# Optimization experiments

Hardware: AMD Instinct MI355X
Metric: run time of the kernel (lower is better)

The kernel has to match this reference:

```python
import jax, jax.numpy as jnp
import numpy as np

N_NODES = 100000
N_EDGES = 1600000
IN_DIM = 128
HID = 128
N_CLASSES = 10
N_GRAPHS = 64


def setup_inputs() -> dict:
    key = jax.random.key(0)
    ks = jax.random.split(key, 12)
    x = jax.random.normal(ks[0], (N_NODES, IN_DIM), dtype=jnp.float32)
    edge_index = jax.random.randint(ks[1], (2, N_EDGES), 0, N_NODES, dtype=jnp.int64)
    batch = jnp.sort(jax.random.randint(ks[2], (N_NODES,), 0, N_GRAPHS, dtype=jnp.int64))
    s = 1.0 / np.sqrt(HID)
    W_gcn = jax.random.uniform(ks[3], (IN_DIM, HID), jnp.float32, -s, s)
    b_gcn = jnp.zeros((HID,), jnp.float32)
    w_ih = jax.random.uniform(ks[4], (4 * HID, HID), jnp.float32, -s, s)
    w_hh = jax.random.uniform(ks[5], (4 * HID, HID), jnp.float32, -s, s)
    b_ih = jax.random.uniform(ks[6], (4 * HID,), jnp.float32, -s, s)
    b_hh = jax.random.uniform(ks[7], (4 * HID,), jnp.float32, -s, s)
    W_fc = jax.random.uniform(ks[8], (N_CLASSES, HID), jnp.float32, -s, s)
    b_fc = jax.random.uniform(ks[9], (N_CLASSES,), jnp.float32, -s, s)
    return dict(x=x, edge_index=edge_index, batch=batch, W_gcn=W_gcn, b_gcn=b_gcn,
                w_ih=w_ih, w_hh=w_hh, b_ih=b_ih, b_hh=b_hh, W_fc=W_fc, b_fc=b_fc)


def _gcn_conv(x, edge_index, W, b):
    # PyG GCNConv: add self-loops, symmetric norm D^-1/2 (A+I) D^-1/2, then bias.
    row, col = edge_index[0], edge_index[1]
    ones = jnp.ones((edge_index.shape[1],), x.dtype)
    deg = jax.ops.segment_sum(ones, col, num_segments=N_NODES) + 1.0  # +1 for self-loop
    dinv = jax.lax.rsqrt(deg)
    xt = x @ W  # [N, HID]
    norm = dinv[row] * dinv[col]  # [E]
    agg = jax.ops.segment_sum(xt[row] * norm[:, None], col, num_segments=N_NODES)
    agg = agg + xt * (dinv * dinv)[:, None]  # self-loop contribution
    return agg + b


def _lstm(seq, w_ih, w_hh, b_ih, b_hh):
    # torch LSTM gate order: i, f, g, o
    def step(carry, x_t):
        h, c = carry
        gates = x_t @ w_ih.T + h @ w_hh.T + b_ih + b_hh
        i, f, g, o = jnp.split(gates, 4)
        c = jax.nn.sigmoid(f) * c + jax.nn.sigmoid(i) * jnp.tanh(g)
        h = jax.nn.sigmoid(o) * jnp.tanh(c)
        return (h, c), h
    h0 = jnp.zeros((HID,), seq.dtype)
    (_, _), hs = jax.lax.scan(step, (h0, h0), seq)
    return hs  # [T, HID]


def reference(x, edge_index, batch, W_gcn, b_gcn, w_ih, w_hh, b_ih, b_hh, W_fc, b_fc):
    h = jax.nn.relu(_gcn_conv(x, edge_index, W_gcn, b_gcn))
    # dropout is identity at inference
    sums = jax.ops.segment_sum(h, batch, num_segments=N_GRAPHS)
    cnt = jax.ops.segment_sum(jnp.ones((N_NODES,), h.dtype), batch, num_segments=N_GRAPHS)
    pooled = sums / jnp.maximum(cnt, 1.0)[:, None]  # [G, HID]
    hs = _lstm(pooled, w_ih, w_hh, b_ih, b_hh)  # [G, HID]
    return hs @ W_fc.T + b_fc  # [G, N_CLASSES]
```

## Files before the change

kernel.cpp:

```cpp
#include <hip/hip_runtime.h>
#include <hip/hip_fp16.h>
#include <math.h>

#if __has_builtin(__builtin_amdgcn_cvt_pk_f32_fp8) && __has_builtin(__builtin_amdgcn_cvt_pk_fp8_f32)
#define HAS_FP8_CVT 1
#else
#include <hip/hip_fp8.h>
#endif

#define NNODES 100000
#define NEDGES 1600000
#define DIM 128
#define NG 64
#define GATE 512
#define SCAN_NB 98
#define FILL_NPASS 4
#define BUCKET ((NNODES + FILL_NPASS - 1) / FILL_NPASS)

#define HG 128
#define HW 25024
#define HSMEM (HW * 4)

#define SMEM_W   131072
#define SMEM_AUX (256 + 2048 + 16384)
#define SMEM_TOTAL (SMEM_W + SMEM_AUX)

typedef _Float16 f16x2 __attribute__((ext_vector_type(2)));
typedef _Float16 half8_t __attribute__((ext_vector_type(8)));
typedef float f32x4 __attribute__((ext_vector_type(4)));
typedef float f32x2_t __attribute__((ext_vector_type(2)));

__device__ __forceinline__ f16x2 f2h2cast(float f) {
    union U { float f; f16x2 h; } u; u.f = f; return u.h;
}
__device__ __forceinline__ float fdot2f(f16x2 a, f16x2 b, float c) {
#if __has_builtin(__builtin_amdgcn_fdot2)
    return __builtin_amdgcn_fdot2(a, b, c, false);
#else
    return c + (float)a[0] * (float)b[0] + (float)a[1] * (float)b[1];
#endif
}

__device__ __forceinline__ unsigned char f32_to_fp8(float v) {
#ifdef HAS_FP8_CVT
    return (unsigned char)(__builtin_amdgcn_cvt_pk_fp8_f32(v, v, 0, false) & 0xFF);
#else
    __hip_fp8_e4m3 h(v); return h.__x;
#endif
}
__device__ __forceinline__ void fp8x4_acc(unsigned w, float* acc) {
#ifdef HAS_FP8_CVT
    f32x2_t lo = __builtin_amdgcn_cvt_pk_f32_fp8((int)w, false);
    f32x2_t hi = __builtin_amdgcn_cvt_pk_f32_fp8((int)w, true);
    acc[0] += lo[0]; acc[1] += lo[1]; acc[2] += hi[0]; acc[3] += hi[1];
#else
    __hip_fp8_e4m3 h;
#pragma unroll
    for (int q = 0; q < 4; ++q) { h.__x = (w >> (8 * q)) & 0xFF; acc[q] += (float)h; }
#endif
}

__device__ __forceinline__ float sigf(float x) {
    return __builtin_amdgcn_rcpf(1.0f + __expf(-x));
}
__device__ __forceinline__ float tanhfast(float x) {
    float e = __expf(2.0f * x);
    return 1.0f - 2.0f * __builtin_amdgcn_rcpf(e + 1.0f);
}

__global__ __launch_bounds__(1024) void k_deghist(const int* __restrict__ ei, unsigned* __restrict__ partial) {
    extern __shared__ unsigned hist[];
    int tid = threadIdx.x;
    for (int i = tid; i < HW; i += 1024) hist[i] = 0u;
    __syncthreads();
    int e0 = blockIdx.x * (NEDGES / HG);
    int e1 = e0 + (NEDGES / HG);
    for (int e = e0 + tid; e < e1; e += 1024) {
        int col = ei[NEDGES + e];
        atomicAdd(&hist[col >> 2], 1u << ((col & 3) * 8));
    }
    __syncthreads();
    unsigned* dst = partial + (size_t)blockIdx.x * HW;
    for (int i = tid; i < HW; i += 1024) dst[i] = hist[i];
}

__global__ __launch_bounds__(256) void k_deg(const int* __restrict__ ei, int* __restrict__ deg) {
    int e = blockIdx.x * 256 + threadIdx.x;
    if (e < NEDGES) atomicAdd(&deg[ei[NEDGES + e]], 1);
}

__global__ __launch_bounds__(256) void k_degred(const unsigned* __restrict__ partial, int* __restrict__ deg,
                                                float* __restrict__ dinv) {
    int w = blockIdx.x * 256 + threadIdx.x;
    if (w >= NNODES / 4) return;
    unsigned s = 0;
    for (int b = 0; b < HG; ++b) s += partial[(size_t)b * HW + w];
    int4 d;
    d.x = s & 255; d.y = (s >> 8) & 255; d.z = (s >> 16) & 255; d.w = (int)(s >> 24);
    ((int4*)deg)[w] = d;
    float4 dv;
    dv.x = rsqrtf((float)d.x + 1.f);
    dv.y = rsqrtf((float)d.y + 1.f);
    dv.z = rsqrtf((float)d.z + 1.f);
    dv.w = rsqrtf((float)d.w + 1.f);
    ((float4*)dinv)[w] = dv;
}

__global__ __launch_bounds__(256) void k_dinv(const int* __restrict__ deg, float* __restrict__ dinv) {
    int n = blockIdx.x * 256 + threadIdx.x;
    if (n < NNODES) dinv[n] = rsqrtf((float)deg[n] + 1.0f);
}

__global__ __launch_bounds__(1024) void k_scan1(const int* __restrict__ deg, int* __restrict__ row_ptr,
                                                int* __restrict__ bsum) {
    __shared__ int ls[1024];
    int tid = threadIdx.x;
    int n = blockIdx.x * 1024 + tid;
    int v = (n < NNODES) ? deg[n] : 0;
    ls[tid] = v;
    __syncthreads();
    for (int off = 1; off < 1024; off <<= 1) {
        int t = (tid >= off) ? ls[tid - off] : 0;
        __syncthreads();
        ls[tid] += t;
        __syncthreads();
    }
    if (n < NNODES) row_ptr[n] = ls[tid] - v;
    if (tid == 1023) bsum[blockIdx.x] = ls[1023];
}

__global__ __launch_bounds__(128) void k_scan2(int* __restrict__ bsum, int* __restrict__ row_ptr,
                                               const int* __restrict__ batch, int* __restrict__ start) {
    __shared__ int ls[128];
    int tid = threadIdx.x;
    int v = (tid < SCAN_NB) ? bsum[tid] : 0;
    ls[tid] = v;
    __syncthreads();
    for (int off = 1; off < 128; off <<= 1) {
        int t = (tid >= off) ? ls[tid - off] : 0;
        __syncthreads();
        ls[tid] += t;
        __syncthreads();
    }
    if (tid < SCAN_NB) bsum[tid] = ls[tid] - v;
    if (tid == 127) row_ptr[NNODES] = ls[127];
    if (tid <= NG) {
        int lo = 0, hi = NNODES;
        while (lo < hi) {
            int mid = (lo + hi) >> 1;
            if (batch[mid] < tid) lo = mid + 1; else hi = mid;
        }
        start[tid] = lo;
    }
}

__global__ __launch_bounds__(1024) void k_scan3(int* __restrict__ row_ptr, const int* __restrict__ bsum,
                                                int* __restrict__ cursor) {
    int n = blockIdx.x * 1024 + threadIdx.x;
    if (n < NNODES) {
        int rp = row_ptr[n] + bsum[blockIdx.x];
        row_ptr[n] = rp;
        cursor[n] = rp;
    }
}

__global__ __launch_bounds__(256) void k_fillb(const int* __restrict__ ei, int* __restrict__ cursor,
                                               int* __restrict__ adj, int b0) {
    int e = blockIdx.x * 256 + threadIdx.x;
    if (e < NEDGES) {
        int col = ei[NEDGES + e];
        if (col >= b0 && col < b0 + BUCKET) {
            int row = ei[e];
            int pos = atomicAdd(&cursor[col], 1);
            adj[pos] = row;
        }
    }
}

__global__ __launch_bounds__(256) void k_wprep(const float* __restrict__ W_gcn, const float* __restrict__ w_hh,
                                               __half* __restrict__ Wt, __half* __restrict__ whh16) {
    int t = blockIdx.x * 256 + threadIdx.x;
    if (t < GATE * DIM) {
        whh16[t] = __float2half(w_hh[t]);
    } else {
        int idx = t - GATE * DIM;
        if (idx < DIM * DIM) {
            int d = idx >> 7, k = idx & 127;
            Wt[idx] = __float2half(W_gcn[k * DIM + d]);
        }
    }
}

__global__ __launch_bounds__(256) void k_gemmm(const float* __restrict__ x, const __half* __restrict__ Wt,
                                               const float* __restrict__ dinv, unsigned char* __restrict__ yf8) {
    int tid = threadIdx.x;
    int wt = tid >> 6, lane = tid & 63;
    int lr = lane & 15, kgrp = lane >> 4;
    int rb = blockIdx.x * 64 + wt * 16;

    int rowA = rb + lr;
    if (rowA >= NNODES) rowA = NNODES - 1;
    const float4* x4 = (const float4*)x;

    f32x4 acc[8];
#pragma unroll
    for (int ct = 0; ct < 8; ++ct) acc[ct] = (f32x4){0.f, 0.f, 0.f, 0.f};

#pragma unroll
    for (int c = 0; c < 4; ++c) {
        int kb = c * 32 + kgrp * 8;
        float4 v0 = x4[(size_t)rowA * 32 + (kb >> 2)];
        float4 v1 = x4[(size_t)rowA * 32 + (kb >> 2) + 1];
        half8_t a;
        a[0] = (_Float16)v0.x; a[1] = (_Float16)v0.y; a[2] = (_Float16)v0.z; a[3] = (_Float16)v0.w;
        a[4] = (_Float16)v1.x; a[5] = (_Float16)v1.y; a[6] = (_Float16)v1.z; a[7] = (_Float16)v1.w;
#pragma unroll
        for (int ct = 0; ct < 8; ++ct) {
            int col = ct * 16 + lr;
            half8_t b = *(const half8_t*)(Wt + (size_t)col * DIM + kb);
            acc[ct] = __builtin_amdgcn_mfma_f32_16x16x32_f16(a, b, acc[ct], 0, 0, 0);
        }
    }

    int rowbase = rb + kgrp * 4;
    float dv[4];
    bool ok[4];
#pragma unroll
    for (int r = 0; r < 4; ++r) {
        int row = rowbase + r;
        ok[r] = row < NNODES;
        dv[r] = ok[r] ? dinv[row] : 0.f;
    }
#pragma unroll
    for (int ct = 0; ct < 8; ++ct) {
#pragma unroll
        for (int r = 0; r < 4; ++r) {
            if (ok[r])
                yf8[(size_t)(rowbase + r) * DIM + ct * 16 + lr] = f32_to_fp8(acc[ct][r] * dv[r]);
        }
    }
}

__global__ __launch_bounds__(256) void k_gpool(const int* __restrict__ row_ptr, const int* __restrict__ adj,
                                               const uint2* __restrict__ Y, const float* __restrict__ dinv,
                                               const float* __restrict__ bias, const int* __restrict__ batch,
                                               float* __restrict__ sums) {
    __shared__ float red[16][132];
    __shared__ int gid[16];
    int tid = threadIdx.x;
    int sl = tid >> 4;
    int l = tid & 15;
    int n = blockIdx.x * 16 + sl;

    int s = row_ptr[n], e = row_ptr[n + 1];
    float acc[8];
#pragma unroll
    for (int q = 0; q < 8; ++q) acc[q] = 0.f;
    {
        uint2 v = Y[(size_t)n * 16 + l];
        fp8x4_acc(v.x, acc);
        fp8x4_acc(v.y, acc + 4);
    }
    int i = s;
    for (; i + 3 < e; i += 4) {
        int r0 = adj[i], r1 = adj[i + 1], r2 = adj[i + 2], r3 = adj[i + 3];
        uint2 a0 = Y[(size_t)r0 * 16 + l];
        uint2 a1 = Y[(size_t)r1 * 16 + l];
        uint2 a2 = Y[(size_t)r2 * 16 + l];
        uint2 a3 = Y[(size_t)r3 * 16 + l];
        fp8x4_acc(a0.x, acc); fp8x4_acc(a0.y, acc + 4);
        fp8x4_acc(a1.x, acc); fp8x4_acc(a1.y, acc + 4);
        fp8x4_acc(a2.x, acc); fp8x4_acc(a2.y, acc + 4);
        fp8x4_acc(a3.x, acc); fp8x4_acc(a3.y, acc + 4);
    }
    for (; i < e; ++i) {
        uint2 a0 = Y[(size_t)adj[i] * 16 + l];
        fp8x4_acc(a0.x, acc); fp8x4_acc(a0.y, acc + 4);
    }

    float dv = dinv[n];
#pragma unroll
    for (int q = 0; q < 8; ++q) {
        float v = dv * acc[q] + bias[l * 8 + q];
        red[sl][l * 8 + q] = fmaxf(v, 0.f);
    }
    if (l == 0) gid[sl] = batch[n];
    __syncthreads();

    if (tid < DIM) {
        int d = tid;
        float a = 0.f;
        int g = gid[0];
        for (int s2 = 0; s2 < 16; ++s2) {
            int gs = gid[s2];
            if (gs != g) {
                if (a != 0.f) atomicAdd(&sums[g * DIM + d], a);
                a = 0.f; g = gs;
            }
            a += red[s2][d];
        }
        if (a != 0.f) atomicAdd(&sums[g * DIM + d], a);
    }
}

__global__ __launch_bounds__(512) void k_xgate(const float* __restrict__ sums, const int* __restrict__ start,
                                               const float* __restrict__ w_ih, const float* __restrict__ b_ih,
                                               const float* __restrict__ b_hh, float* __restrict__ xg) {
    __shared__ float4 p4[DIM / 4];
    int t = blockIdx.x, j = threadIdx.x;
    if (j < DIM) {
        int c = start[t + 1] - start[t];
        float inv = 1.0f / fmaxf((float)c, 1.0f);
        ((float*)p4)[j] = sums[t * DIM + j] * inv;
    }
    __syncthreads();
    const float4* w4 = (const float4*)(w_ih + (size_t)j * DIM);
    float acc = b_ih[j] + b_hh[j];
#pragma unroll
    for (int kk = 0; kk < 32; ++kk) {
        float4 w = w4[kk];
        float4 p = p4[kk];
        acc += w.x * p.x + w.y * p.y + w.z * p.z + w.w * p.w;
    }
    xg[t * GATE + j] = acc;
}

template <int LDSW>
__global__ __launch_bounds__(512) void k_lstm2(const float* __restrict__ xg, const __half* __restrict__ whh16,
                                               const float* __restrict__ Wfc, const float* __restrict__ bfc,
                                               float* __restrict__ out) {
    extern __shared__ char smem[];
    half8_t* w8L = (half8_t*)smem;
    char* aux = LDSW ? (smem + SMEM_W) : smem;
    __half* h2h = (__half*)aux;
    float* gates = (float*)(aux + 256);
    __half* hsh = (__half*)(aux + 256 + 2048);
    int j = threadIdx.x;
    int sw = j & 15;

    if (LDSW) {
#pragma unroll
        for (int c = 0; c < 16; ++c) {
            half8_t g = *(const half8_t*)(whh16 + (size_t)j * DIM + 8 * c);
            w8L[j * 16 + (c ^ sw)] = g;
        }
    }
    if (j < DIM) h2h[j] = __float2half(0.f);
    float c = 0.f;
    float xcur = xg[j];
    __syncthreads();

    const half8_t* wrow = LDSW ? (const half8_t*)w8L : (const half8_t*)whh16;
    const float4* h4 = (const float4*)h2h;
    for (int t = 0; t < NG; ++t) {
        float xnext = (t + 1 < NG) ? xg[(t + 1) * GATE + j] : 0.f;
        float acc = xcur;
#pragma unroll
        for (int cc = 0; cc < 16; ++cc) {
            int idx = LDSW ? (j * 16 + (cc ^ sw)) : (j * 16 + cc);
            union { half8_t v; f16x2 p[4]; } w;
            w.v = wrow[idx];
            float4 hr = h4[cc];
            acc = fdot2f(w.p[0], f2h2cast(hr.x), acc);
            acc = fdot2f(w.p[1], f2h2cast(hr.y), acc);
            acc = fdot2f(w.p[2], f2h2cast(hr.z), acc);
            acc = fdot2f(w.p[3], f2h2cast(hr.w), acc);
        }
        gates[j] = acc;
        __syncthreads();
        if (j < DIM) {
            float gi = gates[j], gf = gates[DIM + j], gg = gates[2 * DIM + j], go = gates[3 * DIM + j];
            c = sigf(gf) * c + sigf(gi) * tanhfast(gg);
            float hn = sigf(go) * tanhfast(c);
            h2h[j] = __float2half(hn);
            hsh[t * DIM + j] = __float2half(hn);
        }
        xcur = xnext;
        __syncthreads();
    }

    for (int o = j; o < NG * 10; o += 512) {
        int t = o / 10, cls = o - t * 10;
        const __half2* hv = (const __half2*)(hsh + t * DIM);
        float acc = bfc[cls];
#pragma unroll
        for (int kk = 0; kk < 64; ++kk) {
            float2 hf = __half22float2(hv[kk]);
            acc += hf.x * Wfc[cls * DIM + 2 * kk] + hf.y * Wfc[cls * DIM + 2 * kk + 1];
        }
        out[o] = acc;
    }
}

extern "C" void kernel_launch(void* const* d_in, const int* in_sizes, int n_in,
                              void* d_out, int out_size, void* d_ws, size_t ws_size,
                              hipStream_t stream) {
    const float* x     = (const float*)d_in[0];
    const int*   ei    = (const int*)d_in[1];
    const int*   batch = (const int*)d_in[2];
    const float* W_gcn = (const float*)d_in[3];
    const float* b_gcn = (const float*)d_in[4];
    const float* w_ih  = (const float*)d_in[5];
    const float* w_hh  = (const float*)d_in[6];
    const float* b_ih  = (const float*)d_in[7];
    const float* b_hh  = (const float*)d_in[8];
    const float* W_fc  = (const float*)d_in[9];
    const float* b_fc  = (const float*)d_in[10];
    float* out = (float*)d_out;

    char* ws = (char*)d_ws;
    unsigned char* yf8 = (unsigned char*)ws;
    __half* wt16  = (__half*)(ws + (size_t)NNODES * DIM * 2);
    unsigned* partial = (unsigned*)(ws + (size_t)NNODES * DIM * 2 + (1 << 16));
    float*  dinv  = (float*)(ws + (size_t)NNODES * DIM * 4);
    float*  sums  = dinv + 100096;
    float*  xg    = sums + NG * DIM;
    int*    deg   = (int*)(xg + NG * GATE);
    int*    row_ptr = deg + 100096;
    int*    cursor  = row_ptr + 100096;
    int*    adj     = cursor + 100096;
    int*    start   = adj + NEDGES;
    int*    bsum    = start + 128;
    __half* whh16   = (__half*)(bsum + 128);

    hipMemsetAsync(sums, 0, NG * DIM * sizeof(float), stream);

    bool hist_ok = hipFuncSetAttribute((const void*)k_deghist,
                                       hipFuncAttributeMaxDynamicSharedMemorySize,
                                       HSMEM) == hipSuccess;
    if (hist_ok) {
        k_deghist<<<HG, 1024, HSMEM, stream>>>(ei, partial);
        k_degred<<<(NNODES / 4 + 255) / 256, 256, 0, stream>>>(partial, deg, dinv);
    } else {
        hipMemsetAsync(deg, 0, NNODES * sizeof(int), stream);
        k_deg<<<(NEDGES + 255) / 256, 256, 0, stream>>>(ei, deg);
        k_dinv<<<(NNODES + 255) / 256, 256, 0, stream>>>(deg, dinv);
    }
    k_scan1<<<SCAN_NB, 1024, 0, stream>>>(deg, row_ptr, bsum);
    k_scan2<<<1, 128, 0, stream>>>(bsum, row_ptr, batch, start);
    k_scan3<<<SCAN_NB, 1024, 0, stream>>>(row_ptr, bsum, cursor);
    for (int p = 0; p < FILL_NPASS; ++p)
        k_fillb<<<(NEDGES + 255) / 256, 256, 0, stream>>>(ei, cursor, adj, p * BUCKET);
    k_wprep<<<(GATE * DIM + DIM * DIM + 255) / 256, 256, 0, stream>>>(W_gcn, w_hh, wt16, whh16);
    k_gemmm<<<(NNODES + 63) / 64, 256, 0, stream>>>(x, wt16, dinv, yf8);
    k_gpool<<<NNODES / 16, 256, 0, stream>>>(row_ptr, adj, (const uint2*)yf8, dinv, b_gcn, batch, sums);
    k_xgate<<<NG, 512, 0, stream>>>(sums, start, w_ih, b_ih, b_hh, xg);

    bool lds_ok = hipFuncSetAttribute((const void*)k_lstm2<1>,
                                      hipFuncAttributeMaxDynamicSharedMemorySize,
                                      SMEM_TOTAL) == hipSuccess;
    if (lds_ok)
        k_lstm2<1><<<1, 512, SMEM_TOTAL, stream>>>(xg, whh16, W_fc, b_fc, out);
    else
        k_lstm2<0><<<1, 512, SMEM_AUX, stream>>>(xg, whh16, W_fc, b_fc, out);
}
```

Before: 283.6 us.

## Replace atomic CSR fill with per-block prefix fill; use MFMA for LSTM recurrence

The degree-reduction kernel now also stores, for each histogram block, an exclusive prefix of the per-block 8-bit degree counts. A new fill kernel uses that prefix plus LDS atomics to place edges into adj, replacing the global cursor atomics. Separately, the single-block LSTM recurrence switches from fdot2 over LDS-staged weights to 16x16x32 f16 MFMA, with w_hh held in registers and h broadcast as row 0 of the A matrix. This removes global atomic contention and the serial dot-product latency, at the cost of wasted MFMA rows and extra workspace traffic for pre8.

Result: faster. 236.2 us (-16.7%).

```diff
diff --git a/kernel.cpp b/kernel.cpp
--- a/kernel.cpp
+++ b/kernel.cpp
@@ -21,25 +21,9 @@
 #define HW 25024
 #define HSMEM (HW * 4)
 
-#define SMEM_W   131072
-#define SMEM_AUX (256 + 2048 + 16384)
-#define SMEM_TOTAL (SMEM_W + SMEM_AUX)
-
-typedef _Float16 f16x2 __attribute__((ext_vector_type(2)));
 typedef _Float16 half8_t __attribute__((ext_vector_type(8)));
 typedef float f32x4 __attribute__((ext_vector_type(4)));
 typedef float f32x2_t __attribute__((ext_vector_type(2)));
-
-__device__ __forceinline__ f16x2 f2h2cast(float f) {
-    union U { float f; f16x2 h; } u; u.f = f; return u.h;
-}
-__device__ __forceinline__ float fdot2f(f16x2 a, f16x2 b, float c) {
-#if __has_builtin(__builtin_amdgcn_fdot2)
-    return __builtin_amdgcn_fdot2(a, b, c, false);
-#else
-    return c + (float)a[0] * (float)b[0] + (float)a[1] * (float)b[1];
-#endif
-}
 
 __device__ __forceinline__ unsigned char f32_to_fp8(float v) {
 #ifdef HAS_FP8_CVT
@@ -89,12 +73,15 @@
     if (e < NEDGES) atomicAdd(&deg[ei[NEDGES + e]], 1);
 }
 
-__global__ __launch_bounds__(256) void k_degred(const unsigned* __restrict__ partial, int* __restrict__ deg,
-                                                float* __restrict__ dinv) {
+__global__ __launch_bounds__(256) void k_degred2(const unsigned* __restrict__ partial, unsigned* __restrict__ pre8,
+                                                 int* __restrict__ deg, float* __restrict__ dinv) {
     int w = blockIdx.x * 256 + threadIdx.x;
     if (w >= NNODES / 4) return;
     unsigned s = 0;
-    for (int b = 0; b < HG; ++b) s += partial[(size_t)b * HW + w];
+    for (int b = 0; b < HG; ++b) {
+        pre8[(size_t)b * HW + w] = s;
+        s += partial[(size_t)b * HW + w];
+    }
     int4 d;
     d.x = s & 255; d.y = (s >> 8) & 255; d.z = (s >> 16) & 255; d.w = (int)(s >> 24);
     ((int4*)deg)[w] = d;
@@ -161,6 +148,28 @@
         int rp = row_ptr[n] + bsum[blockIdx.x];
         row_ptr[n] = rp;
         cursor[n] = rp;
+    }
+}
+
+__global__ __launch_bounds__(1024) void k_fill2(const int* __restrict__ ei, const int* __restrict__ row_ptr,
+                                                const unsigned* __restrict__ pre8, int* __restrict__ adj, int b0) {
+    __shared__ unsigned lh[BUCKET / 4];
+    int tid = threadIdx.x;
+    for (int i = tid; i < BUCKET / 4; i += 1024) lh[i] = 0u;
+    __syncthreads();
+    const unsigned* myPre = pre8 + (size_t)blockIdx.x * HW;
+    int e0 = blockIdx.x * (NEDGES / HG);
+    int e1 = e0 + (NEDGES / HG);
+    for (int e = e0 + tid; e < e1; e += 1024) {
+        int col = ei[NEDGES + e];
+        if (col >= b0 && col < b0 + BUCKET) {
+            int row = ei[e];
+            int lc = col - b0;
+            unsigned old = atomicAdd(&lh[lc >> 2], 1u << ((lc & 3) * 8));
+            int local = (old >> ((lc & 3) * 8)) & 0xFF;
+            int base = row_ptr[col] + (int)((myPre[col >> 2] >> ((col & 3) * 8)) & 0xFF);
+            adj[base + local] = row;
+        }
     }
 }
 
@@ -325,61 +334,70 @@
     xg[t * GATE + j] = acc;
 }
 
-template <int LDSW>
-__global__ __launch_bounds__(512) void k_lstm2(const float* __restrict__ xg, const __half* __restrict__ whh16,
+__global__ __launch_bounds__(512) void k_lstmm(const float* __restrict__ xg, const __half* __restrict__ whh16,
                                                const float* __restrict__ Wfc, const float* __restrict__ bfc,
                                                float* __restrict__ out) {
-    extern __shared__ char smem[];
-    half8_t* w8L = (half8_t*)smem;
-    char* aux = LDSW ? (smem + SMEM_W) : smem;
-    __half* h2h = (__half*)aux;
-    float* gates = (float*)(aux + 256);
-    __half* hsh = (__half*)(aux + 256 + 2048);
-    int j = threadIdx.x;
-    int sw = j & 15;
-
-    if (LDSW) {
-#pragma unroll
-        for (int c = 0; c < 16; ++c) {
-            half8_t g = *(const half8_t*)(whh16 + (size_t)j * DIM + 8 * c);
-            w8L[j * 16 + (c ^ sw)] = g;
-        }
-    }
-    if (j < DIM) h2h[j] = __float2half(0.f);
+    __shared__ __half h2h[DIM];
+    __shared__ float gates[GATE];
+    __shared__ __half hsh[NG * DIM];
+    int tid = threadIdx.x;
+    int wid = tid >> 6, lane = tid & 63;
+    int lr = lane & 15, kg = lane >> 4;
+    int colbase = wid * 64;
+
+    half8_t bf[4][4];
+#pragma unroll
+    for (int ct = 0; ct < 4; ++ct)
+#pragma unroll
+        for (int ks = 0; ks < 4; ++ks)
+            bf[ct][ks] = *(const half8_t*)(whh16 + (size_t)(colbase + ct * 16 + lr) * DIM + ks * 32 + kg * 8);
+
+    if (tid < DIM) h2h[tid] = __float2half(0.f);
     float c = 0.f;
-    float xcur = xg[j];
-    __syncthreads();
-
-    const half8_t* wrow = LDSW ? (const half8_t*)w8L : (const half8_t*)whh16;
-    const float4* h4 = (const float4*)h2h;
+    float xc[4], xn[4];
+#pragma unroll
+    for (int ct = 0; ct < 4; ++ct) xc[ct] = xg[colbase + ct * 16 + lr];
+    __syncthreads();
+
     for (int t = 0; t < NG; ++t) {
-        float xnext = (t + 1 < NG) ? xg[(t + 1) * GATE + j] : 0.f;
-        float acc = xcur;
-#pragma unroll
-        for (int cc = 0; cc < 16; ++cc) {
-            int idx = LDSW ? (j * 16 + (cc ^ sw)) : (j * 16 + cc);
-            union { half8_t v; f16x2 p[4]; } w;
-            w.v = wrow[idx];
-            float4 hr = h4[cc];
-            acc = fdot2f(w.p[0], f2h2cast(hr.x), acc);
-            acc = fdot2f(w.p[1], f2h2cast(hr.y), acc);
-            acc = fdot2f(w.p[2], f2h2cast(hr.z), acc);
-            acc = fdot2f(w.p[3], f2h2cast(hr.w), acc);
-        }
-        gates[j] = acc;
-        __syncthreads();
-        if (j < DIM) {
-            float gi = gates[j], gf = gates[DIM + j], gg = gates[2 * DIM + j], go = gates[3 * DIM + j];
+        half8_t a[4];
+#pragma unroll
+        for (int ks = 0; ks < 4; ++ks) {
+            half8_t av = {};
+            if (lr == 0) av = *(const half8_t*)(h2h + ks * 32 + kg * 8);
+            a[ks] = av;
+        }
+        f32x4 acc[4];
+#pragma unroll
+        for (int ct = 0; ct < 4; ++ct) {
+            f32x4 z = (f32x4){0.f, 0.f, 0.f, 0.f};
+            if (lane < 16) z[0] = xc[ct];
+            acc[ct] = z;
+#pragma unroll
+            for (int ks = 0; ks < 4; ++ks)
+                acc[ct] = __builtin_amdgcn_mfma_f32_16x16x32_f16(a[ks], bf[ct][ks], acc[ct], 0, 0, 0);
+        }
+        int tn = (t + 1 < NG) ? t + 1 : t;
+#pragma unroll
+        for (int ct = 0; ct < 4; ++ct) xn[ct] = xg[tn * GATE + colbase + ct * 16 + lr];
+        if (lane < 16) {
+#pragma unroll
+            for (int ct = 0; ct < 4; ++ct) gates[colbase + ct * 16 + lane] = acc[ct][0];
+        }
+        __syncthreads();
+        if (tid < DIM) {
+            float gi = gates[tid], gf = gates[DIM + tid], gg = gates[2 * DIM + tid], go = gates[3 * DIM + tid];
             c = sigf(gf) * c + sigf(gi) * tanhfast(gg);
             float hn = sigf(go) * tanhfast(c);
-            h2h[j] = __float2half(hn);
-            hsh[t * DIM + j] = __float2half(hn);
-        }
-        xcur = xnext;
-        __syncthreads();
-    }
-
-    for (int o = j; o < NG * 10; o += 512) {
+            h2h[tid] = __float2half(hn);
+            hsh[t * DIM + tid] = __float2half(hn);
+        }
+#pragma unroll
+        for (int ct = 0; ct < 4; ++ct) xc[ct] = xn[ct];
+        __syncthreads();
+    }
+
+    for (int o = tid; o < NG * 10; o += 512) {
         int t = o / 10, cls = o - t * 10;
         const __half2* hv = (const __half2*)(hsh + t * DIM);
         float acc = bfc[cls];
@@ -410,6 +428,7 @@
 
     char* ws = (char*)d_ws;
     unsigned char* yf8 = (unsigned char*)ws;
+    unsigned* pre8 = (unsigned*)(ws + (size_t)NNODES * DIM);
     __half* wt16  = (__half*)(ws + (size_t)NNODES * DIM * 2);
     unsigned* partial = (unsigned*)(ws + (size_t)NNODES * DIM * 2 + (1 << 16));
     float*  dinv  = (float*)(ws + (size_t)NNODES * DIM * 4);
@@ -430,7 +449,7 @@
                                        HSMEM) == hipSuccess;
     if (hist_ok) {
         k_deghist<<<HG, 1024, HSMEM, stream>>>(ei, partial);
-        k_degred<<<(NNODES / 4 + 255) / 256, 256, 0, stream>>>(partial, deg, dinv);
+        k_degred2<<<(NNODES / 4 + 255) / 256, 256, 0, stream>>>(partial, pre8, deg, dinv);
     } else {
         hipMemsetAsync(deg, 0, NNODES * sizeof(int), stream);
         k_deg<<<(NEDGES + 255) / 256, 256, 0, stream>>>(ei, deg);
@@ -439,18 +458,16 @@
     k_scan1<<<SCAN_NB, 1024, 0, stream>>>(deg, row_ptr, bsum);
     k_scan2<<<1, 128, 0, stream>>>(bsum, row_ptr, batch, start);
     k_scan3<<<SCAN_NB, 1024, 0, stream>>>(row_ptr, bsum, cursor);
-    for (int p = 0; p < FILL_NPASS; ++p)
-        k_fillb<<<(NEDGES + 255) / 256, 256, 0, stream>>>(ei, cursor, adj, p * BUCKET);
+    if (hist_ok) {
+        for (int p = 0; p < FILL_NPASS; ++p)
+            k_fill2<<<HG, 1024, 0, stream>>>(ei, row_ptr, pre8, adj, p * BUCKET);
+    } else {
+        for (int p = 0; p < FILL_NPASS; ++p)
+            k_fillb<<<(NEDGES + 255) / 256, 256, 0, stream>>>(ei, cursor, adj, p * BUCKET);
+    }
     k_wprep<<<(GATE * DIM + DIM * DIM + 255) / 256, 256, 0, stream>>>(W_gcn, w_hh, wt16, whh16);
     k_gemmm<<<(NNODES + 63) / 64, 256, 0, stream>>>(x, wt16, dinv, yf8);
     k_gpool<<<NNODES / 16, 256, 0, stream>>>(row_ptr, adj, (const uint2*)yf8, dinv, b_gcn, batch, sums);
     k_xgate<<<NG, 512, 0, stream>>>(sums, start, w_ih, b_ih, b_hh, xg);
-
-    bool lds_ok = hipFuncSetAttribute((const void*)k_lstm2<1>,
-                                      hipFuncAttributeMaxDynamicSharedMemorySize,
-                                      SMEM_TOTAL) == hipSuccess;
-    if (lds_ok)
-        k_lstm2<1><<<1, 512, SMEM_TOTAL, stream>>>(xg, whh16, W_fc, b_fc, out);
-    else
-        k_lstm2<0><<<1, 512, SMEM_AUX, stream>>>(xg, whh16, W_fc, b_fc, out);
-}
+    k_lstmm<<<1, 512, 0, stream>>>(xg, whh16, W_fc, b_fc, out);
+}
```
